# Kernel tuning notes

Measured on AMD Instinct MI355X. Metric: run time of the kernel, lower is better.

Reference implementation:

```python
import jax, jax.numpy as jnp
import numpy as np

N = 50000        # nodes
E = 800000       # edges (before self-loops)
A_DIM = 128      # attribute dim (= a_hid)
S_DIM = 64       # structural dim (= s_hid)
L = 4            # num_layers


def setup_inputs() -> dict:
    key = jax.random.key(0)
    ks = jax.random.split(key, 10)
    sc = 0.05
    return {
        "x": jax.random.normal(ks[0], (N, A_DIM), jnp.float32),
        "s": jax.random.normal(ks[1], (N, S_DIM), jnp.float32),
        "edge_index": jax.random.randint(ks[2], (2, E), 0, N, dtype=jnp.int64),
        "gcn_W": jax.random.normal(ks[3], (L, A_DIM, A_DIM), jnp.float32) * sc,
        "gcn_b": jnp.zeros((L, A_DIM), jnp.float32),
        "gna_w1W": jax.random.normal(ks[4], (L, S_DIM, S_DIM), jnp.float32) * sc,
        "gna_w1b": jnp.zeros((L, S_DIM), jnp.float32),
        "gna_w2W": jax.random.normal(ks[5], (L, S_DIM, S_DIM), jnp.float32) * sc,
        "gna_w2b": jnp.zeros((L, S_DIM), jnp.float32),
        "gna_a": jax.random.normal(ks[6], (L, S_DIM), jnp.float32) * sc,
    }


def _gelu(v):
    return jax.nn.gelu(v, approximate=False)  # matches torch F.gelu default


def _self_loops(edge_index, n):
    loop = jnp.arange(n, dtype=edge_index.dtype)
    row = jnp.concatenate([edge_index[0], loop])  # src
    col = jnp.concatenate([edge_index[1], loop])  # dst
    return row, col


def _guide_forward(x, s, edge_index, gcn_W, gcn_b,
                   gna_w1W, gna_w1b, gna_w2W, gna_w2b, gna_a):
    n = x.shape[0]
    row, col = _self_loops(edge_index, n)  # [E+N]

    # ---- attribute autoencoder: GCN with symmetric normalization ----
    deg = jax.ops.segment_sum(jnp.ones_like(col, dtype=x.dtype), col, num_segments=n)
    dinv = jnp.where(deg > 0, jax.lax.rsqrt(deg), 0.0)
    norm = dinv[row] * dinv[col]                       # [E+N]
    h = x
    for i in range(L):
        h2 = h @ gcn_W[i]                              # [N, A]
        agg = jax.ops.segment_sum(norm[:, None] * h2[row], col, num_segments=n)
        h = agg + gcn_b[i]
        if i < L - 1:                                  # jk=None: no act after last
            h = _gelu(h)

    # ---- structure autoencoder: GNA with edge-softmax attention ----
    g = s
    for i in range(L):
        t = g @ gna_w2W[i] + gna_w2b[i]                # w2(s), [N, S]
        # alpha_e = (t_dst - t_src) @ a, softmax over edges grouped by dst
        alpha = (t[col] - t[row]) @ gna_a[i]           # [E+N]
        amax = jax.ops.segment_max(alpha, col, num_segments=n)
        e = jnp.exp(alpha - amax[col])
        denom = jax.ops.segment_sum(e, col, num_segments=n)
        w = e / (denom[col] + 1e-16)
        msg = jax.ops.segment_sum(w[:, None] * t[row], col, num_segments=n)
        out = g @ gna_w1W[i] + gna_w1b[i] + msg
        g = _gelu(out)                                 # act applied after every layer
    return h, g


def reference(x, s, edge_index, gcn_W, gcn_b,
              gna_w1W, gna_w1b, gna_w2W, gna_w2b, gna_a):
    return _guide_forward(x, s, edge_index, gcn_W, gcn_b,
                          gna_w1W, gna_w1b, gna_w2W, gna_w2b, gna_a)
```

## Files before the change

kernel.cpp:

```cpp
#include <hip/hip_runtime.h>
#include <hip/hip_fp16.h>
#include <math.h>

#define N_NODES 50000
#define E_EDGES 800000
#define ET (E_EDGES + N_NODES)
#define L_LAYERS 4
#define NB_SCAN ((N_NODES + 255) / 256)
#define MF_BLOCKS ((N_NODES + 63) / 64)
#define WAVE_BLOCKS ((N_NODES * 64 + 255) / 256)

typedef __attribute__((ext_vector_type(8))) short short8;
typedef __attribute__((ext_vector_type(4))) float f32x4;

__device__ __forceinline__ float gelu_f(float x) {
    return 0.5f * x * (1.0f + erff(x * 0.70710678118654752f));
}

__device__ __forceinline__ void split_hl(float x, unsigned short& h, unsigned short& lo) {
    unsigned u = __float_as_uint(x);
    h = (unsigned short)(u >> 16);
    float hif = __uint_as_float(u & 0xffff0000u);
    lo = (unsigned short)(__float_as_uint(x - hif) >> 16);
}

__device__ __forceinline__ void fma8h(const float4& raw, float m, float* acc) {
    const __half2* h = reinterpret_cast<const __half2*>(&raw);
#pragma unroll
    for (int i = 0; i < 4; ++i) {
        float2 f = __half22float2(h[i]);
        acc[2 * i]     = fmaf(f.x, m, acc[2 * i]);
        acc[2 * i + 1] = fmaf(f.y, m, acc[2 * i + 1]);
    }
}


__global__ __launch_bounds__(256) void count_pos(const int* __restrict__ ecol,
                                                 int* __restrict__ cnt,
                                                 int* __restrict__ aux) {
    int e = blockIdx.x * 256 + threadIdx.x;
    if (e >= ET) return;
    int c = (e < E_EDGES) ? ecol[e] : (e - E_EDGES);
    aux[e] = atomicAdd(&cnt[c], 1);
}

__global__ __launch_bounds__(256) void scan_part1(const int* __restrict__ cnt,
                                                  int* __restrict__ bsum) {
    __shared__ int red[256];
    int t = threadIdx.x;
    int i = blockIdx.x * 256 + t;
    red[t] = (i < N_NODES) ? cnt[i] : 0;
    __syncthreads();
#pragma unroll
    for (int off = 128; off; off >>= 1) {
        if (t < off) red[t] += red[t + off];
        __syncthreads();
    }
    if (t == 0) bsum[blockIdx.x] = red[0];
}

__global__ __launch_bounds__(256) void scan_part2(int* __restrict__ bsum) {
    __shared__ int sh[256];
    int t = threadIdx.x;
    int v = (t < NB_SCAN) ? bsum[t] : 0;
    sh[t] = v;
    __syncthreads();
    for (int off = 1; off < 256; off <<= 1) {
        int u = (t >= off) ? sh[t - off] : 0;
        __syncthreads();
        sh[t] += u;
        __syncthreads();
    }
    if (t < NB_SCAN) bsum[t] = sh[t] - v;
}

__global__ __launch_bounds__(256) void scan_part3(const int* __restrict__ cnt,
                                                  const int* __restrict__ bsum,
                                                  int* __restrict__ ptrb,
                                                  float* __restrict__ dinv) {
    __shared__ int sh[256];
    int t = threadIdx.x;
    int i = blockIdx.x * 256 + t;
    int v = (i < N_NODES) ? cnt[i] : 0;
    sh[t] = v;
    __syncthreads();
    for (int off = 1; off < 256; off <<= 1) {
        int u = (t >= off) ? sh[t - off] : 0;
        __syncthreads();
        sh[t] += u;
        __syncthreads();
    }
    int excl = sh[t] - v + bsum[blockIdx.x];
    if (i < N_NODES) {
        ptrb[i] = excl;
        dinv[i] = rsqrtf((float)v);
    }
    if (i == N_NODES - 1) ptrb[N_NODES] = excl + v;
}

__global__ __launch_bounds__(256) void bucket(const int* __restrict__ erow,
                                              const int* __restrict__ ecol,
                                              const int* __restrict__ aux,
                                              const int* __restrict__ ptrb,
                                              int* __restrict__ eidx) {
    int e = blockIdx.x * 256 + threadIdx.x;
    if (e >= ET) return;
    int r, c;
    if (e < E_EDGES) { r = erow[e]; c = ecol[e]; }
    else             { r = e - E_EDGES; c = r; }
    int pos = ptrb[c] + aux[e];
    eidx[pos] = r;
}


__global__ __launch_bounds__(256) void prep_w(const float* __restrict__ gcn_W,
                                              const float* __restrict__ w1W,
                                              const float* __restrict__ w2W,
                                              unsigned short* __restrict__ gf_hi,
                                              unsigned short* __restrict__ gf_lo,
                                              unsigned short* __restrict__ nf_hi,
                                              unsigned short* __restrict__ nf_lo) {
    int idx = blockIdx.x * 256 + threadIdx.x;
    if (idx < 8192) {
        int lane = idx & 63, nt = (idx >> 6) & 7, s = (idx >> 9) & 3, layer = idx >> 11;
        int q = lane >> 4, n = lane & 15;
        const float* W = gcn_W + (size_t)layer * 128 * 128;
        size_t o = (size_t)idx * 8;
#pragma unroll
        for (int j = 0; j < 8; ++j) {
            float x = W[(size_t)(s * 32 + q * 8 + j) * 128 + nt * 16 + n];
            unsigned short h, lo;
            split_hl(x, h, lo);
            gf_hi[o + j] = h; gf_lo[o + j] = lo;
        }
    } else if (idx < 8192 + 4096) {
        int t = idx - 8192;
        int lane = t & 63, nt = (t >> 6) & 7, s = (t >> 9) & 1, layer = t >> 10;
        int q = lane >> 4, n = lane & 15;
        int col = nt * 16 + n;
        const float* W = (col < 64) ? (w1W + (size_t)layer * 64 * 64)
                                    : (w2W + (size_t)layer * 64 * 64);
        int c = col & 63;
        size_t o = (size_t)t * 8;
#pragma unroll
        for (int j = 0; j < 8; ++j) {
            float x = W[(size_t)(s * 32 + q * 8 + j) * 64 + c];
            unsigned short h, lo;
            split_hl(x, h, lo);
            nf_hi[o + j] = h; nf_lo[o + j] = lo;
        }
    }
}


__device__ __forceinline__ void mfma_steps(const float* __restrict__ A, int Kfull,
                                           int nsteps,
                                           const unsigned short* __restrict__ wfh,
                                           const unsigned short* __restrict__ wfl,
                                           int arow, bool avalid, int lq, int l,
                                           f32x4* acc) {
    for (int s = 0; s < nsteps; ++s) {
        float4 a0 = make_float4(0.f, 0.f, 0.f, 0.f);
        float4 a1 = make_float4(0.f, 0.f, 0.f, 0.f);
        if (avalid) {
            const float* ap = A + (size_t)arow * Kfull + s * 32 + lq * 8;
            a0 = *(const float4*)ap;
            a1 = *(const float4*)(ap + 4);
        }
        float xs[8] = {a0.x, a0.y, a0.z, a0.w, a1.x, a1.y, a1.z, a1.w};
        short8 ah, al;
#pragma unroll
        for (int c = 0; c < 8; ++c) {
            unsigned short h, lo;
            split_hl(xs[c], h, lo);
            ah[c] = (short)h; al[c] = (short)lo;
        }
#pragma unroll
        for (int nt = 0; nt < 8; ++nt) {
            size_t fo = ((size_t)(s * 8 + nt) * 64 + l) * 8;
            short8 wh = *(const short8*)(wfh + fo);
            short8 wl = *(const short8*)(wfl + fo);
            acc[nt] = __builtin_amdgcn_mfma_f32_16x16x32_bf16(ah, wh, acc[nt], 0, 0, 0);
            acc[nt] = __builtin_amdgcn_mfma_f32_16x16x32_bf16(ah, wl, acc[nt], 0, 0, 0);
            acc[nt] = __builtin_amdgcn_mfma_f32_16x16x32_bf16(al, wh, acc[nt], 0, 0, 0);
        }
    }
}


__global__ __launch_bounds__(256) void gemm_both(
    const float* __restrict__ A0, const float* __restrict__ A1,
    const unsigned short* __restrict__ gfh, const unsigned short* __restrict__ gfl,
    const unsigned short* __restrict__ nfh, const unsigned short* __restrict__ nfl,
    const float* __restrict__ b1, const float* __restrict__ b2,
    const float* __restrict__ avec, const float* __restrict__ dinv,
    __half* __restrict__ h2, float* __restrict__ baseb,
    __half* __restrict__ ut, float* __restrict__ ub) {
    int tid = threadIdx.x;
    int w  = tid >> 6;
    int l  = tid & 63;
    int lq = l >> 4;
    int ln = l & 15;
    bool isg = blockIdx.x >= MF_BLOCKS;
    int blk = isg ? (blockIdx.x - MF_BLOCKS) : blockIdx.x;
    int m0 = blk * 64;
    int arow = m0 + w * 16 + ln;
    bool avalid = arow < N_NODES;

    f32x4 acc[8];
#pragma unroll
    for (int i = 0; i < 8; ++i) acc[i] = (f32x4){0.f, 0.f, 0.f, 0.f};

    if (!isg) {
        mfma_steps(A0, 128, 4, gfh, gfl, arow, avalid, lq, l, acc);
        float dv[4];
#pragma unroll
        for (int r = 0; r < 4; ++r) {
            int row = m0 + w * 16 + lq * 4 + r;
            dv[r] = (row < N_NODES) ? dinv[row] : 0.f;
        }
#pragma unroll
        for (int nt = 0; nt < 8; ++nt) {
            int col = nt * 16 + ln;
#pragma unroll
            for (int r = 0; r < 4; ++r) {
                int row = m0 + w * 16 + lq * 4 + r;
                if (row < N_NODES)
                    h2[(size_t)row * 128 + col] = __float2half(acc[nt][r] * dv[r]);
            }
        }
    } else {
        mfma_steps(A1, 64, 2, nfh, nfl, arow, avalid, lq, l, acc);
#pragma unroll
        for (int nt = 0; nt < 4; ++nt) {
            int col = nt * 16 + ln;
            float bb = b1[col];
#pragma unroll
            for (int r = 0; r < 4; ++r) {
                int row = m0 + w * 16 + lq * 4 + r;
                if (row < N_NODES) baseb[(size_t)row * 64 + col] = acc[nt][r] + bb;
            }
        }
        float pa[4] = {0.f, 0.f, 0.f, 0.f};
        float t2s[4][4];
#pragma unroll
        for (int nt = 4; nt < 8; ++nt) {
            int col = (nt - 4) * 16 + ln;
            float bb = b2[col];
            float av = avec[col];
#pragma unroll
            for (int r = 0; r < 4; ++r) {
                float t2 = acc[nt][r] + bb;
                t2s[nt - 4][r] = t2;
                pa[r] += t2 * av;
            }
        }
#pragma unroll
        for (int r = 0; r < 4; ++r) {
            pa[r] += __shfl_xor(pa[r], 1);
            pa[r] += __shfl_xor(pa[r], 2);
            pa[r] += __shfl_xor(pa[r], 4);
            pa[r] += __shfl_xor(pa[r], 8);
        }
        float ur[4];
#pragma unroll
        for (int r = 0; r < 4; ++r) ur[r] = expf(-pa[r]);
#pragma unroll
        for (int nt = 0; nt < 4; ++nt) {
            int col = nt * 16 + ln;
#pragma unroll
            for (int r = 0; r < 4; ++r) {
                int row = m0 + w * 16 + lq * 4 + r;
                if (row < N_NODES)
                    ut[(size_t)row * 64 + col] = __float2half(t2s[nt][r] * ur[r]);
            }
        }
        if (ln == 0) {
#pragma unroll
            for (int r = 0; r < 4; ++r) {
                int row = m0 + w * 16 + lq * 4 + r;
                if (row < N_NODES) ub[row] = ur[r];
            }
        }
    }
}


__global__ __launch_bounds__(256) void agg_gcn(const __half* __restrict__ h2,
                                               const int* __restrict__ ptrb,
                                               const int* __restrict__ eidx,
                                               const float* __restrict__ dinv,
                                               const float* __restrict__ bias,
                                               float* __restrict__ out,
                                               int apply_gelu) {
    int dst  = (blockIdx.x * 256 + threadIdx.x) >> 6;
    int lane = threadIdx.x & 63;
    if (dst >= N_NODES) return;
    int sub = lane >> 4;
    int fl  = lane & 15;
    int p0 = ptrb[dst], p1 = ptrb[dst + 1];
    float acc[8];
#pragma unroll
    for (int i = 0; i < 8; ++i) acc[i] = 0.f;
    for (int p = p0; p < p1; p += 64) {
        int nb = min(64, p1 - p);
        int srcs = (lane < nb) ? eidx[p + lane] : 0;
        for (int eb = 0; eb < nb; eb += 16) {
            int   sv[4];
            float mk[4];
#pragma unroll
            for (int k = 0; k < 4; ++k) {
                int e = eb + sub + 4 * k;
                int c = min(e, nb - 1);
                sv[k] = __shfl(srcs, c);
                mk[k] = (e < nb) ? 1.f : 0.f;
            }
            float4 raw[4];
#pragma unroll
            for (int k = 0; k < 4; ++k)
                raw[k] = *(const float4*)(h2 + (size_t)sv[k] * 128 + fl * 8);
#pragma unroll
            for (int k = 0; k < 4; ++k) fma8h(raw[k], mk[k], acc);
        }
    }
#pragma unroll
    for (int off = 16; off <= 32; off <<= 1)
#pragma unroll
        for (int i = 0; i < 8; ++i) acc[i] += __shfl_xor(acc[i], off);
    if (sub == 0) {
        float dd = dinv[dst];
        float4 b0 = *(const float4*)(bias + fl * 8);
        float4 b1v = *(const float4*)(bias + fl * 8 + 4);
        float bb[8] = {b0.x, b0.y, b0.z, b0.w, b1v.x, b1v.y, b1v.z, b1v.w};
        float vo[8];
#pragma unroll
        for (int i = 0; i < 8; ++i) {
            float v = fmaf(dd, acc[i], bb[i]);
            vo[i] = apply_gelu ? gelu_f(v) : v;
        }
        *(float4*)(out + (size_t)dst * 128 + fl * 8) =
            make_float4(vo[0], vo[1], vo[2], vo[3]);
        *(float4*)(out + (size_t)dst * 128 + fl * 8 + 4) =
            make_float4(vo[4], vo[5], vo[6], vo[7]);
    }
}


__global__ __launch_bounds__(256) void gna_agg(const __half* __restrict__ ut,
                                               const float* __restrict__ ub,
                                               const int* __restrict__ ptrb,
                                               const int* __restrict__ eidx,
                                               const float* __restrict__ base,
                                               float* __restrict__ gout) {
    int dst  = (blockIdx.x * 256 + threadIdx.x) >> 6;
    int lane = threadIdx.x & 63;
    if (dst >= N_NODES) return;
    int p0 = ptrb[dst], p1 = ptrb[dst + 1];
    int sub = lane >> 3;
    int fl  = lane & 7;
    float se = 0.f;
    float acc[8];
#pragma unroll
    for (int i = 0; i < 8; ++i) acc[i] = 0.f;
    for (int p = p0; p < p1; p += 64) {
        int nb = min(64, p1 - p);
        int srcs = (lane < nb) ? eidx[p + lane] : 0;
        if (lane < nb) se += ub[srcs];
        for (int eb = 0; eb < nb; eb += 32) {
            int   sv[4];
            float mk[4];
#pragma unroll
            for (int k = 0; k < 4; ++k) {
                int e = eb + sub + 8 * k;
                int c = min(e, nb - 1);
                sv[k] = __shfl(srcs, c);
                mk[k] = (e < nb) ? 1.f : 0.f;
            }
            float4 raw[4];
#pragma unroll
            for (int k = 0; k < 4; ++k)
                raw[k] = *(const float4*)(ut + (size_t)sv[k] * 64 + fl * 8);
#pragma unroll
            for (int k = 0; k < 4; ++k) fma8h(raw[k], mk[k], acc);
        }
    }
#pragma unroll
    for (int off = 1; off < 64; off <<= 1) se += __shfl_xor(se, off);
#pragma unroll
    for (int off = 8; off <= 32; off <<= 1)
#pragma unroll
        for (int i = 0; i < 8; ++i) acc[i] += __shfl_xor(acc[i], off);
    if (sub == 0) {
        float winv = 1.0f / (se + 1e-16f);
        float4 s0 = *(const float4*)(base + (size_t)dst * 64 + fl * 8);
        float4 s1 = *(const float4*)(base + (size_t)dst * 64 + fl * 8 + 4);
        float bs[8] = {s0.x, s0.y, s0.z, s0.w, s1.x, s1.y, s1.z, s1.w};
        float vo[8];
#pragma unroll
        for (int i = 0; i < 8; ++i)
            vo[i] = gelu_f(fmaf(acc[i], winv, bs[i]));
        *(float4*)(gout + (size_t)dst * 64 + fl * 8) =
            make_float4(vo[0], vo[1], vo[2], vo[3]);
        *(float4*)(gout + (size_t)dst * 64 + fl * 8 + 4) =
            make_float4(vo[4], vo[5], vo[6], vo[7]);
    }
}


extern "C" void kernel_launch(void* const* d_in, const int* in_sizes, int n_in,
                              void* d_out, int out_size, void* d_ws, size_t ws_size,
                              hipStream_t stream) {
    const float* x     = (const float*)d_in[0];
    const float* s     = (const float*)d_in[1];
    const int*   ei    = (const int*)d_in[2];
    const float* gcn_W = (const float*)d_in[3];
    const float* gcn_b = (const float*)d_in[4];
    const float* w1W   = (const float*)d_in[5];
    const float* w1b   = (const float*)d_in[6];
    const float* w2W   = (const float*)d_in[7];
    const float* w2b   = (const float*)d_in[8];
    const float* ga    = (const float*)d_in[9];

    float* h_out = (float*)d_out;
    float* g_out = (float*)d_out + (size_t)N_NODES * 128;

    size_t off = 0;
    char* wsb = (char*)d_ws;
    auto take = [&](size_t bytes) {
        void* p = wsb + off;
        off = (off + bytes + 255) & ~(size_t)255;
        return p;
    };
    int*    cnt     = (int*)take((size_t)N_NODES * 4);
    int*    ptrb    = (int*)take((size_t)(N_NODES + 1) * 4);
    int*    aux     = (int*)take((size_t)ET * 4);
    float*  dinv    = (float*)take((size_t)N_NODES * 4);
    int*    eidx    = (int*)take((size_t)ET * 4);
    __half* h2      = (__half*)take((size_t)N_NODES * 128 * 2);
    __half* utbuf   = (__half*)take((size_t)N_NODES * 64 * 2);
    float*  basebuf = (float*)take((size_t)N_NODES * 64 * 4);
    float*  ubuf    = (float*)take((size_t)N_NODES * 4);
    int*    bsum    = (int*)take((size_t)NB_SCAN * 4);
    unsigned short* gf_hi = (unsigned short*)take((size_t)8192 * 8 * 2);
    unsigned short* gf_lo = (unsigned short*)take((size_t)8192 * 8 * 2);
    unsigned short* nf_hi = (unsigned short*)take((size_t)4096 * 8 * 2);
    unsigned short* nf_lo = (unsigned short*)take((size_t)4096 * 8 * 2);
    (void)ws_size; (void)in_sizes; (void)n_in; (void)out_size;

    const int* erow = ei;
    const int* ecol = ei + E_EDGES;

    hipMemsetAsync(cnt, 0, (size_t)N_NODES * 4, stream);

    int ge = (ET + 255) / 256;
    count_pos<<<ge, 256, 0, stream>>>(ecol, cnt, aux);
    scan_part1<<<NB_SCAN, 256, 0, stream>>>(cnt, bsum);
    scan_part2<<<1, 256, 0, stream>>>(bsum);
    scan_part3<<<NB_SCAN, 256, 0, stream>>>(cnt, bsum, ptrb, dinv);
    bucket<<<ge, 256, 0, stream>>>(erow, ecol, aux, ptrb, eidx);
    prep_w<<<48, 256, 0, stream>>>(gcn_W, w1W, w2W, gf_hi, gf_lo, nf_hi, nf_lo);

    const float* hin = x;
    const float* gin = s;
    for (int l = 0; l < L_LAYERS; ++l) {
        gemm_both<<<2 * MF_BLOCKS, 256, 0, stream>>>(
            hin, gin,
            gf_hi + (size_t)l * 4 * 8 * 64 * 8, gf_lo + (size_t)l * 4 * 8 * 64 * 8,
            nf_hi + (size_t)l * 2 * 8 * 64 * 8, nf_lo + (size_t)l * 2 * 8 * 64 * 8,
            w1b + (size_t)l * 64, w2b + (size_t)l * 64, ga + (size_t)l * 64, dinv,
            h2, basebuf, utbuf, ubuf);
        agg_gcn<<<WAVE_BLOCKS, 256, 0, stream>>>(
            h2, ptrb, eidx, dinv, gcn_b + (size_t)l * 128, h_out,
            (l < L_LAYERS - 1) ? 1 : 0);
        gna_agg<<<WAVE_BLOCKS, 256, 0, stream>>>(
            utbuf, ubuf, ptrb, eidx, basebuf, g_out);
        hin = h_out;
        gin = g_out;
    }
}
```

Baseline: 507.7 us.

## Fuse GCN and GNA aggregation kernels, fold scan pass, use fast GELU

Merges the two per-layer aggregation kernels into one launch, where the block index picks the GCN or GNA body. This removes a launch and lets the two independent gathers overlap. It also drops the single-block scan kernel: each scan_part3 block now reduces the preceding block sums itself. GELU switches from erff to an Abramowitz-Stegun polynomial with __expf, and the softmax reciprocal uses __fdividef. Both trade a small amount of accuracy for cheaper math.

```diff
diff --git a/kernel.cpp b/kernel.cpp
--- a/kernel.cpp
+++ b/kernel.cpp
@@ -14,7 +14,14 @@
 typedef __attribute__((ext_vector_type(4))) float f32x4;
 
 __device__ __forceinline__ float gelu_f(float x) {
-    return 0.5f * x * (1.0f + erff(x * 0.70710678118654752f));
+    float z = fabsf(x) * 0.70710678118654752f;
+    float t = __fdividef(1.0f, fmaf(0.3275911f, z, 1.0f));
+    float p = t * fmaf(t, fmaf(t, fmaf(t, fmaf(t, 1.061405429f, -1.453152027f),
+                                       1.421413741f), -0.284496736f),
+                       0.254829592f);
+    float e = __expf(-z * z);
+    float erfz = copysignf(fmaf(-p, e, 1.0f), x);
+    return 0.5f * x * (1.0f + erfz);
 }
 
 __device__ __forceinline__ void split_hl(float x, unsigned short& h, unsigned short& lo) {
@@ -59,27 +66,21 @@
     if (t == 0) bsum[blockIdx.x] = red[0];
 }
 
-__global__ __launch_bounds__(256) void scan_part2(int* __restrict__ bsum) {
-    __shared__ int sh[256];
-    int t = threadIdx.x;
-    int v = (t < NB_SCAN) ? bsum[t] : 0;
-    sh[t] = v;
-    __syncthreads();
-    for (int off = 1; off < 256; off <<= 1) {
-        int u = (t >= off) ? sh[t - off] : 0;
-        __syncthreads();
-        sh[t] += u;
-        __syncthreads();
-    }
-    if (t < NB_SCAN) bsum[t] = sh[t] - v;
-}
-
 __global__ __launch_bounds__(256) void scan_part3(const int* __restrict__ cnt,
                                                   const int* __restrict__ bsum,
                                                   int* __restrict__ ptrb,
                                                   float* __restrict__ dinv) {
+    __shared__ int red[256];
     __shared__ int sh[256];
     int t = threadIdx.x;
+    red[t] = (t < (int)blockIdx.x) ? bsum[t] : 0;
+    __syncthreads();
+#pragma unroll
+    for (int off = 128; off; off >>= 1) {
+        if (t < off) red[t] += red[t + off];
+        __syncthreads();
+    }
+    int base = red[0];
     int i = blockIdx.x * 256 + t;
     int v = (i < N_NODES) ? cnt[i] : 0;
     sh[t] = v;
@@ -90,7 +91,7 @@
         sh[t] += u;
         __syncthreads();
     }
-    int excl = sh[t] - v + bsum[blockIdx.x];
+    int excl = sh[t] - v + base;
     if (i < N_NODES) {
         ptrb[i] = excl;
         dinv[i] = rsqrtf((float)v);
@@ -286,16 +287,14 @@
 }
 
 
-__global__ __launch_bounds__(256) void agg_gcn(const __half* __restrict__ h2,
-                                               const int* __restrict__ ptrb,
-                                               const int* __restrict__ eidx,
-                                               const float* __restrict__ dinv,
-                                               const float* __restrict__ bias,
-                                               float* __restrict__ out,
-                                               int apply_gelu) {
-    int dst  = (blockIdx.x * 256 + threadIdx.x) >> 6;
-    int lane = threadIdx.x & 63;
-    if (dst >= N_NODES) return;
+__device__ __forceinline__ void gcn_body(int dst, int lane,
+                                         const __half* __restrict__ h2,
+                                         const int* __restrict__ ptrb,
+                                         const int* __restrict__ eidx,
+                                         const float* __restrict__ dinv,
+                                         const float* __restrict__ bias,
+                                         float* __restrict__ out,
+                                         int apply_gelu) {
     int sub = lane >> 4;
     int fl  = lane & 15;
     int p0 = ptrb[dst], p1 = ptrb[dst + 1];
@@ -345,16 +344,13 @@
     }
 }
 
-
-__global__ __launch_bounds__(256) void gna_agg(const __half* __restrict__ ut,
-                                               const float* __restrict__ ub,
-                                               const int* __restrict__ ptrb,
-                                               const int* __restrict__ eidx,
-                                               const float* __restrict__ base,
-                                               float* __restrict__ gout) {
-    int dst  = (blockIdx.x * 256 + threadIdx.x) >> 6;
-    int lane = threadIdx.x & 63;
-    if (dst >= N_NODES) return;
+__device__ __forceinline__ void gna_body(int dst, int lane,
+                                         const __half* __restrict__ ut,
+                                         const float* __restrict__ ub,
+                                         const int* __restrict__ ptrb,
+                                         const int* __restrict__ eidx,
+                                         const float* __restrict__ base,
+                                         float* __restrict__ gout) {
     int p0 = ptrb[dst], p1 = ptrb[dst + 1];
     int sub = lane >> 3;
     int fl  = lane & 7;
@@ -391,7 +387,7 @@
 #pragma unroll
         for (int i = 0; i < 8; ++i) acc[i] += __shfl_xor(acc[i], off);
     if (sub == 0) {
-        float winv = 1.0f / (se + 1e-16f);
+        float winv = __fdividef(1.0f, se + 1e-16f);
         float4 s0 = *(const float4*)(base + (size_t)dst * 64 + fl * 8);
         float4 s1 = *(const float4*)(base + (size_t)dst * 64 + fl * 8 + 4);
         float bs[8] = {s0.x, s0.y, s0.z, s0.w, s1.x, s1.y, s1.z, s1.w};
@@ -404,6 +400,23 @@
         *(float4*)(gout + (size_t)dst * 64 + fl * 8 + 4) =
             make_float4(vo[4], vo[5], vo[6], vo[7]);
     }
+}
+
+__global__ __launch_bounds__(256) void agg_both(
+    const __half* __restrict__ h2, const int* __restrict__ ptrb,
+    const int* __restrict__ eidx, const float* __restrict__ dinv,
+    const float* __restrict__ gcn_bias, float* __restrict__ h_out, int apply_gelu,
+    const __half* __restrict__ ut, const float* __restrict__ ub,
+    const float* __restrict__ baseb, float* __restrict__ g_out) {
+    int lane = threadIdx.x & 63;
+    bool isg = blockIdx.x >= WAVE_BLOCKS;
+    int blk = isg ? (blockIdx.x - WAVE_BLOCKS) : blockIdx.x;
+    int dst = (blk * 256 + (int)threadIdx.x) >> 6;
+    if (dst >= N_NODES) return;
+    if (!isg)
+        gcn_body(dst, lane, h2, ptrb, eidx, dinv, gcn_bias, h_out, apply_gelu);
+    else
+        gna_body(dst, lane, ut, ub, ptrb, eidx, baseb, g_out);
 }
 
 
@@ -455,7 +468,6 @@
     int ge = (ET + 255) / 256;
     count_pos<<<ge, 256, 0, stream>>>(ecol, cnt, aux);
     scan_part1<<<NB_SCAN, 256, 0, stream>>>(cnt, bsum);
-    scan_part2<<<1, 256, 0, stream>>>(bsum);
     scan_part3<<<NB_SCAN, 256, 0, stream>>>(cnt, bsum, ptrb, dinv);
     bucket<<<ge, 256, 0, stream>>>(erow, ecol, aux, ptrb, eidx);
     prep_w<<<48, 256, 0, stream>>>(gcn_W, w1W, w2W, gf_hi, gf_lo, nf_hi, nf_lo);
@@ -469,11 +481,10 @@
             nf_hi + (size_t)l * 2 * 8 * 64 * 8, nf_lo + (size_t)l * 2 * 8 * 64 * 8,
             w1b + (size_t)l * 64, w2b + (size_t)l * 64, ga + (size_t)l * 64, dinv,
             h2, basebuf, utbuf, ubuf);
-        agg_gcn<<<WAVE_BLOCKS, 256, 0, stream>>>(
+        agg_both<<<2 * WAVE_BLOCKS, 256, 0, stream>>>(
             h2, ptrb, eidx, dinv, gcn_b + (size_t)l * 128, h_out,
-            (l < L_LAYERS - 1) ? 1 : 0);
-        gna_agg<<<WAVE_BLOCKS, 256, 0, stream>>>(
-            utbuf, ubuf, ptrb, eidx, basebuf, g_out);
+            (l < L_LAYERS - 1) ? 1 : 0,
+            utbuf, ubuf, basebuf, g_out);
         hin = h_out;
         gin = g_out;
     }
```

Result: slower. 522.1 us (+2.8%).
